# Optimization experiments

Measured on AMD Instinct MI355X. Metric: run time of the kernel, lower is better.

Reference implementation:

```python
import jax, jax.numpy as jnp
import numpy as np

N, DIM, H, E = 50000, 64, 8, 800000
NEG_SLOPE = 0.2


def setup_inputs() -> dict:
    key = jax.random.key(0)
    ks = jax.random.split(key, 6)
    x = jax.random.normal(ks[0], (N, DIM), dtype=jnp.float32)
    edge_index = jax.random.randint(ks[1], (2, E), 0, N, dtype=jnp.int32)
    # glorot-ish scaled params
    W = jax.random.normal(ks[2], (DIM, H * DIM), dtype=jnp.float32) * (1.0 / np.sqrt(DIM))
    att_src = jax.random.normal(ks[3], (H, DIM), dtype=jnp.float32) * (1.0 / np.sqrt(DIM))
    att_dst = jax.random.normal(ks[4], (H, DIM), dtype=jnp.float32) * (1.0 / np.sqrt(DIM))
    bias = jnp.zeros((DIM,), dtype=jnp.float32)
    return {"x": x, "edge_index": edge_index, "W": W, "att_src": att_src, "att_dst": att_dst, "bias": bias}


def reference(x, edge_index, W, att_src, att_dst, bias):
    n = x.shape[0]
    # PyG GATConv default: add self-loops
    loops = jnp.arange(n, dtype=edge_index.dtype)
    src = jnp.concatenate([edge_index[0], loops])  # [E+N]
    dst = jnp.concatenate([edge_index[1], loops])  # [E+N]
    # project: [N, H, C]
    h = (x @ W).reshape(n, H, DIM)
    # per-node attention contributions: [N, H]
    a_src = jnp.einsum("nhc,hc->nh", h, att_src)
    a_dst = jnp.einsum("nhc,hc->nh", h, att_dst)
    # per-edge logits with LeakyReLU: [E+N, H]
    logits = jax.nn.leaky_relu(a_src[src] + a_dst[dst], negative_slope=NEG_SLOPE)
    # segment softmax over incoming edges of each destination node
    seg_max = jax.ops.segment_max(logits, dst, num_segments=n)  # [N, H]
    seg_max = jnp.where(jnp.isfinite(seg_max), seg_max, 0.0)
    e = jnp.exp(logits - seg_max[dst])
    denom = jax.ops.segment_sum(e, dst, num_segments=n)  # [N, H]
    alpha = e / denom[dst]  # every node has a self-loop -> denom > 0
    # weighted messages and scatter-add: [E+N, H, C] -> [N, H, C]
    msg = h[src] * alpha[:, :, None]
    out = jax.ops.segment_sum(msg, dst, num_segments=n)
    # concat=False -> mean over heads, then bias
    return out.mean(axis=1) + bias
```

## Files before the change

### kernel.cpp

```cpp
#include <hip/hip_runtime.h>
#include <hip/hip_bf16.h>

#define NHEAD 8
#define KDIM 64
#define NCOL 512
#define NEG_SLOPE 0.2f
#define BUCKET 64
#define EPT 8

typedef short bf16x8 __attribute__((ext_vector_type(8)));
typedef float f32x4 __attribute__((ext_vector_type(4)));

__device__ inline float leaky(float x) { return fmaxf(x, NEG_SLOPE * x); }
__device__ inline float bf2f(unsigned short u) { return __uint_as_float(((unsigned)u) << 16); }
__device__ inline unsigned short f2bf(float f) {
    unsigned b = __float_as_uint(f);
    b += 0x7FFFu + ((b >> 16) & 1u);
    return (unsigned short)(b >> 16);
}

__global__ void k_wprep(const float* __restrict__ W, const float* __restrict__ att_src,
                        const float* __restrict__ att_dst,
                        float* __restrict__ WsT, float* __restrict__ WdT,
                        unsigned short* __restrict__ Bhi, unsigned short* __restrict__ Blo) {
    int tid = blockIdx.x * 256 + threadIdx.x;
    if (tid < NHEAD * KDIM) {
        int h = tid >> 6, k = tid & 63;
        float ps = 0.f, pd = 0.f;
        const float4* wp = (const float4*)(W + (size_t)k * NCOL + h * KDIM);
        const float4* sp = (const float4*)(att_src + h * KDIM);
        const float4* dp = (const float4*)(att_dst + h * KDIM);
        #pragma unroll
        for (int q = 0; q < KDIM / 4; ++q) {
            float4 wv = wp[q], sv = sp[q], dv = dp[q];
            ps += wv.x * sv.x + wv.y * sv.y + wv.z * sv.z + wv.w * sv.w;
            pd += wv.x * dv.x + wv.y * dv.y + wv.z * dv.z + wv.w * dv.w;
        }
        WsT[h * KDIM + k] = ps;
        WdT[h * KDIM + k] = pd;
    }
    if (tid < 4 * 16 * 64 * 8) {
        int j  = tid & 7;
        int l  = (tid >> 3) & 63;
        int kk = (tid >> 9) & 15;
        int ct = tid >> 13;
        int c  = ct * 16 + (l & 15);
        int hk = kk * 32 + ((l >> 4) << 3) + j;
        int h = hk >> 6, kx = hk & 63;
        float w = W[(size_t)kx * NCOL + h * KDIM + c];
        unsigned short hi = f2bf(w);
        Bhi[tid] = hi;
        Blo[tid] = f2bf(w - bf2f(hi));
    }
}

__global__ void k_xafill(const float* __restrict__ x,
                         const int* __restrict__ src, const int* __restrict__ dst,
                         const float* __restrict__ WsT, const float* __restrict__ WdT,
                         float* __restrict__ asrc, float* __restrict__ adst,
                         unsigned short* __restrict__ xb,
                         int* __restrict__ cur, unsigned short* __restrict__ bucket,
                         int n, int E, int nbx) {
    const int b = blockIdx.x;
    const int t = threadIdx.x;
    if (b < nbx) {
        int i = b * 256 + t;
        if (i >= n * NHEAD) return;
        int node = i >> 3, h = i & 7;
        const float4* xp = (const float4*)(x + (size_t)node * KDIM);
        const float4* sp = (const float4*)(WsT + h * KDIM);
        const float4* dp = (const float4*)(WdT + h * KDIM);
        float ps = 0.f, pd = 0.f;
        float4 kept0 = {0, 0, 0, 0}, kept1 = {0, 0, 0, 0};
        #pragma unroll
        for (int q = 0; q < KDIM / 4; ++q) {
            float4 xv = xp[q], sv = sp[q], dv = dp[q];
            if (q == 2 * h)     kept0 = xv;
            if (q == 2 * h + 1) kept1 = xv;
            ps += xv.x * sv.x + xv.y * sv.y + xv.z * sv.z + xv.w * sv.w;
            pd += xv.x * dv.x + xv.y * dv.y + xv.z * dv.z + xv.w * dv.w;
        }
        asrc[i] = ps;
        adst[i] = pd;
        ushort4 o0, o1;
        o0.x = f2bf(kept0.x); o0.y = f2bf(kept0.y); o0.z = f2bf(kept0.z); o0.w = f2bf(kept0.w);
        o1.x = f2bf(kept1.x); o1.y = f2bf(kept1.y); o1.z = f2bf(kept1.z); o1.w = f2bf(kept1.w);
        ushort4* op = (ushort4*)(xb + (size_t)node * KDIM + h * 8);
        op[0] = o0; op[1] = o1;
    } else {
        long long base = ((long long)(b - nbx) * 256 + t) * EPT;
        if (base + EPT <= E) {
            int4 d0 = *(const int4*)(dst + base);
            int4 d1 = *(const int4*)(dst + base + 4);
            int4 s0 = *(const int4*)(src + base);
            int4 s1 = *(const int4*)(src + base + 4);
            int dd[EPT] = {d0.x, d0.y, d0.z, d0.w, d1.x, d1.y, d1.z, d1.w};
            int ss[EPT] = {s0.x, s0.y, s0.z, s0.w, s1.x, s1.y, s1.z, s1.w};
            int pp[EPT];
            #pragma unroll
            for (int q = 0; q < EPT; ++q) pp[q] = atomicAdd(cur + dd[q], 1);
            #pragma unroll
            for (int q = 0; q < EPT; ++q)
                if (pp[q] < BUCKET)
                    bucket[(size_t)dd[q] * BUCKET + pp[q]] = (unsigned short)ss[q];
        } else {
            for (long long i = base; i < E; ++i) {
                int d = dst[i];
                int p = atomicAdd(cur + d, 1);
                if (p < BUCKET) bucket[(size_t)d * BUCKET + p] = (unsigned short)src[i];
            }
        }
    }
}

__global__ __launch_bounds__(256, 8) void k_aggproj(const unsigned short* __restrict__ bucket,
                                                    const int* __restrict__ cur,
                                                    const float* __restrict__ asrc,
                                                    const float* __restrict__ adst,
                                                    const unsigned short* __restrict__ xb,
                                                    const unsigned short* __restrict__ Bhi,
                                                    const unsigned short* __restrict__ Blo,
                                                    const float* __restrict__ bias,
                                                    float* __restrict__ out, int n) {
    __shared__ __align__(16) unsigned short Yh_l[16][520];

    const int t = threadIdx.x;
    const int w = t >> 6;
    const int lane = t & 63;
    const int base = blockIdx.x * 16;
    const int hg = lane >> 3;
    const int dly = (lane & 7) << 3;

    for (int q = 0; q < 4; ++q) {
        const int row = w * 4 + q;
        int d = base + row;
        if (d >= n) d = n - 1;

        const float myAd = adst[(size_t)d * NHEAD + hg];
        float den = 0.f;
        float y[8];
        #pragma unroll
        for (int i = 0; i < 8; ++i) y[i] = 0.f;

#define PROCU(AV, RW)                                                          \
    {                                                                          \
        float e_ = __expf(leaky((AV) + myAd));                                 \
        den += e_;                                                             \
        uint4 u_ = (RW);                                                       \
        y[0] += e_ * __uint_as_float(u_.x << 16);                              \
        y[1] += e_ * __uint_as_float(u_.x & 0xFFFF0000u);                      \
        y[2] += e_ * __uint_as_float(u_.y << 16);                              \
        y[3] += e_ * __uint_as_float(u_.y & 0xFFFF0000u);                      \
        y[4] += e_ * __uint_as_float(u_.z << 16);                              \
        y[5] += e_ * __uint_as_float(u_.z & 0xFFFF0000u);                      \
        y[6] += e_ * __uint_as_float(u_.w << 16);                              \
        y[7] += e_ * __uint_as_float(u_.w & 0xFFFF0000u);                      \
    }

        int cnt = cur[d];
        cnt = cnt < BUCKET ? cnt : BUCKET;
        int sv = (lane < cnt) ? (int)bucket[(size_t)d * BUCKET + lane] : 0;

        {
            float a = asrc[(size_t)d * NHEAD + hg];
            uint4 r = *(const uint4*)(xb + ((size_t)d << 6) + dly);
            PROCU(a, r)
        }

        int j = 0;
        for (; j + 4 <= cnt; j += 4) {
            int s0 = __shfl(sv, j);
            int s1 = __shfl(sv, j + 1);
            int s2 = __shfl(sv, j + 2);
            int s3 = __shfl(sv, j + 3);
            float a0 = asrc[(size_t)s0 * NHEAD + hg];
            float a1 = asrc[(size_t)s1 * NHEAD + hg];
            float a2 = asrc[(size_t)s2 * NHEAD + hg];
            float a3 = asrc[(size_t)s3 * NHEAD + hg];
            uint4 r0 = *(const uint4*)(xb + ((size_t)s0 << 6) + dly);
            uint4 r1 = *(const uint4*)(xb + ((size_t)s1 << 6) + dly);
            uint4 r2 = *(const uint4*)(xb + ((size_t)s2 << 6) + dly);
            uint4 r3 = *(const uint4*)(xb + ((size_t)s3 << 6) + dly);
            PROCU(a0, r0)
            PROCU(a1, r1)
            PROCU(a2, r2)
            PROCU(a3, r3)
        }
        for (; j < cnt; ++j) {
            int s = __shfl(sv, j);
            float a = asrc[(size_t)s * NHEAD + hg];
            uint4 r = *(const uint4*)(xb + ((size_t)s << 6) + dly);
            PROCU(a, r)
        }
#undef PROCU

        float inv = 1.0f / den;
        ushort4 h0, h1;
        h0.x = f2bf(y[0] * inv); h0.y = f2bf(y[1] * inv);
        h0.z = f2bf(y[2] * inv); h0.w = f2bf(y[3] * inv);
        h1.x = f2bf(y[4] * inv); h1.y = f2bf(y[5] * inv);
        h1.z = f2bf(y[6] * inv); h1.w = f2bf(y[7] * inv);
        unsigned short* yh = &Yh_l[row][hg * KDIM + dly];
        ((ushort4*)yh)[0] = h0; ((ushort4*)yh)[1] = h1;
    }

    __syncthreads();

    const bf16x8* BH = (const bf16x8*)Bhi;
    const bf16x8* BL = (const bf16x8*)Blo;
    const int ar = lane & 15;
    const int ak = (lane >> 4) << 3;

    f32x4 acc = {0.f, 0.f, 0.f, 0.f};
    #pragma unroll
    for (int kk = 0; kk < 16; ++kk) {
        bf16x8 ah = *(const bf16x8*)&Yh_l[ar][kk * 32 + ak];
        bf16x8 bh = BH[(w * 16 + kk) * 64 + lane];
        bf16x8 bl = BL[(w * 16 + kk) * 64 + lane];
        acc = __builtin_amdgcn_mfma_f32_16x16x32_bf16(ah, bh, acc, 0, 0, 0);
        acc = __builtin_amdgcn_mfma_f32_16x16x32_bf16(ah, bl, acc, 0, 0, 0);
    }

    int col = w * 16 + (lane & 15);
    float b = bias[col];
    int rbase = base + ((lane >> 4) << 2);
    #pragma unroll
    for (int r = 0; r < 4; ++r) {
        int rowg = rbase + r;
        if (rowg < n) out[(size_t)rowg * KDIM + col] = acc[r] * 0.125f + b;
    }
}

extern "C" void kernel_launch(void* const* d_in, const int* in_sizes, int n_in,
                              void* d_out, int out_size, void* d_ws, size_t ws_size,
                              hipStream_t stream) {
    const float* x       = (const float*)d_in[0];
    const int*   ei      = (const int*)d_in[1];
    const float* W       = (const float*)d_in[2];
    const float* att_src = (const float*)d_in[3];
    const float* att_dst = (const float*)d_in[4];
    const float* bias    = (const float*)d_in[5];

    const int n = in_sizes[0] / KDIM;
    const int E = in_sizes[1] / 2;
    const int* src = ei;
    const int* dst = ei + E;

    char* w = (char*)d_ws;
    unsigned short* xb  = (unsigned short*)w;  w += (size_t)n * KDIM * 2;
    unsigned short* Bhi = (unsigned short*)w;  w += (size_t)32768 * 2;
    unsigned short* Blo = (unsigned short*)w;  w += (size_t)32768 * 2;
    float* WsT  = (float*)w;                   w += (size_t)NHEAD * KDIM * 4;
    float* WdT  = (float*)w;                   w += (size_t)NHEAD * KDIM * 4;
    float* asrc = (float*)w;                   w += (size_t)n * NHEAD * 4;
    float* adst = (float*)w;                   w += (size_t)n * NHEAD * 4;
    int*   cur  = (int*)w;                     w += (size_t)n * 4;
    unsigned short* bucket = (unsigned short*)w; w += (size_t)n * BUCKET * 2;

    hipMemsetAsync(cur, 0, (size_t)n * 4, stream);

    k_wprep<<<128, 256, 0, stream>>>(W, att_src, att_dst, WsT, WdT, Bhi, Blo);

    const int nbx = (n * NHEAD + 255) / 256;
    const int ethreads = (E + EPT - 1) / EPT;
    const int nbe = (ethreads + 255) / 256;
    k_xafill<<<nbx + nbe, 256, 0, stream>>>(x, src, dst, WsT, WdT, asrc, adst, xb,
                                            cur, bucket, n, E, nbx);

    k_aggproj<<<(n + 15) / 16, 256, 0, stream>>>(bucket, cur, asrc, adst, xb, Bhi, Blo,
                                                 bias, (float*)d_out, n);
}
```

Measured before the change: 156.6 us.

## Fold counter reset into weight prep, dedupe exp per edge, store x as fp16

Removes the separate memset by zeroing the per-node counters inside the weight-prep kernel. The aggregation loop now computes one exp per (edge, head) across lanes and broadcasts it with shuffles, instead of every lane recomputing it for its head. The loop is also unrolled to 8 edges. The gathered x rows are stored as fp16 instead of bf16, which changes the rounding of the messages and adds half-to-float conversions.

```diff
diff --git a/kernel.cpp b/kernel.cpp
--- a/kernel.cpp
+++ b/kernel.cpp
@@ -1,5 +1,6 @@
 #include <hip/hip_runtime.h>
 #include <hip/hip_bf16.h>
+#include <hip/hip_fp16.h>
 
 #define NHEAD 8
 #define KDIM 64
@@ -22,8 +23,10 @@
 __global__ void k_wprep(const float* __restrict__ W, const float* __restrict__ att_src,
                         const float* __restrict__ att_dst,
                         float* __restrict__ WsT, float* __restrict__ WdT,
-                        unsigned short* __restrict__ Bhi, unsigned short* __restrict__ Blo) {
+                        unsigned short* __restrict__ Bhi, unsigned short* __restrict__ Blo,
+                        int* __restrict__ cur, int n) {
     int tid = blockIdx.x * 256 + threadIdx.x;
+    for (int i = tid; i < n; i += 32768) cur[i] = 0;
     if (tid < NHEAD * KDIM) {
         int h = tid >> 6, k = tid & 63;
         float ps = 0.f, pd = 0.f;
@@ -83,8 +86,14 @@
         asrc[i] = ps;
         adst[i] = pd;
         ushort4 o0, o1;
-        o0.x = f2bf(kept0.x); o0.y = f2bf(kept0.y); o0.z = f2bf(kept0.z); o0.w = f2bf(kept0.w);
-        o1.x = f2bf(kept1.x); o1.y = f2bf(kept1.y); o1.z = f2bf(kept1.z); o1.w = f2bf(kept1.w);
+        o0.x = __half_as_ushort(__float2half_rn(kept0.x));
+        o0.y = __half_as_ushort(__float2half_rn(kept0.y));
+        o0.z = __half_as_ushort(__float2half_rn(kept0.z));
+        o0.w = __half_as_ushort(__float2half_rn(kept0.w));
+        o1.x = __half_as_ushort(__float2half_rn(kept1.x));
+        o1.y = __half_as_ushort(__float2half_rn(kept1.y));
+        o1.z = __half_as_ushort(__float2half_rn(kept1.z));
+        o1.w = __half_as_ushort(__float2half_rn(kept1.w));
         ushort4* op = (ushort4*)(xb + (size_t)node * KDIM + h * 8);
         op[0] = o0; op[1] = o1;
     } else {
@@ -129,70 +138,92 @@
     const int lane = t & 63;
     const int base = blockIdx.x * 16;
     const int hg = lane >> 3;
+    const int hLo = lane & 7;
     const int dly = (lane & 7) << 3;
+
+#define PROCU(EV, RW)                                                          \
+    {                                                                          \
+        den += (EV);                                                           \
+        const __half* hx_ = (const __half*)&(RW);                              \
+        y[0] = fmaf(__half2float(hx_[0]), (EV), y[0]);                         \
+        y[1] = fmaf(__half2float(hx_[1]), (EV), y[1]);                         \
+        y[2] = fmaf(__half2float(hx_[2]), (EV), y[2]);                         \
+        y[3] = fmaf(__half2float(hx_[3]), (EV), y[3]);                         \
+        y[4] = fmaf(__half2float(hx_[4]), (EV), y[4]);                         \
+        y[5] = fmaf(__half2float(hx_[5]), (EV), y[5]);                         \
+        y[6] = fmaf(__half2float(hx_[6]), (EV), y[6]);                         \
+        y[7] = fmaf(__half2float(hx_[7]), (EV), y[7]);                         \
+    }
 
     for (int q = 0; q < 4; ++q) {
         const int row = w * 4 + q;
         int d = base + row;
         if (d >= n) d = n - 1;
 
-        const float myAd = adst[(size_t)d * NHEAD + hg];
+        const float adLo = adst[(size_t)d * NHEAD + hLo];
         float den = 0.f;
         float y[8];
         #pragma unroll
         for (int i = 0; i < 8; ++i) y[i] = 0.f;
 
-#define PROCU(AV, RW)                                                          \
-    {                                                                          \
-        float e_ = __expf(leaky((AV) + myAd));                                 \
-        den += e_;                                                             \
-        uint4 u_ = (RW);                                                       \
-        y[0] += e_ * __uint_as_float(u_.x << 16);                              \
-        y[1] += e_ * __uint_as_float(u_.x & 0xFFFF0000u);                      \
-        y[2] += e_ * __uint_as_float(u_.y << 16);                              \
-        y[3] += e_ * __uint_as_float(u_.y & 0xFFFF0000u);                      \
-        y[4] += e_ * __uint_as_float(u_.z << 16);                              \
-        y[5] += e_ * __uint_as_float(u_.z & 0xFFFF0000u);                      \
-        y[6] += e_ * __uint_as_float(u_.w << 16);                              \
-        y[7] += e_ * __uint_as_float(u_.w & 0xFFFF0000u);                      \
-    }
-
         int cnt = cur[d];
         cnt = cnt < BUCKET ? cnt : BUCKET;
         int sv = (lane < cnt) ? (int)bucket[(size_t)d * BUCKET + lane] : 0;
 
         {
-            float a = asrc[(size_t)d * NHEAD + hg];
+            float asLo = asrc[(size_t)d * NHEAD + hLo];
+            float evs = __expf(leaky(asLo + adLo));
+            float e = __shfl(evs, hg);
             uint4 r = *(const uint4*)(xb + ((size_t)d << 6) + dly);
-            PROCU(a, r)
+            PROCU(e, r)
         }
 
         int j = 0;
-        for (; j + 4 <= cnt; j += 4) {
+        for (; j + 8 <= cnt; j += 8) {
+            int sb = __shfl(sv, j + (lane >> 3));
+            float ab = asrc[(size_t)sb * NHEAD + hLo];
+            float ev = __expf(leaky(ab + adLo));
             int s0 = __shfl(sv, j);
             int s1 = __shfl(sv, j + 1);
             int s2 = __shfl(sv, j + 2);
             int s3 = __shfl(sv, j + 3);
-            float a0 = asrc[(size_t)s0 * NHEAD + hg];
-            float a1 = asrc[(size_t)s1 * NHEAD + hg];
-            float a2 = asrc[(size_t)s2 * NHEAD + hg];
-            float a3 = asrc[(size_t)s3 * NHEAD + hg];
+            int s4 = __shfl(sv, j + 4);
+            int s5 = __shfl(sv, j + 5);
+            int s6 = __shfl(sv, j + 6);
+            int s7 = __shfl(sv, j + 7);
             uint4 r0 = *(const uint4*)(xb + ((size_t)s0 << 6) + dly);
             uint4 r1 = *(const uint4*)(xb + ((size_t)s1 << 6) + dly);
             uint4 r2 = *(const uint4*)(xb + ((size_t)s2 << 6) + dly);
             uint4 r3 = *(const uint4*)(xb + ((size_t)s3 << 6) + dly);
-            PROCU(a0, r0)
-            PROCU(a1, r1)
-            PROCU(a2, r2)
-            PROCU(a3, r3)
+            uint4 r4 = *(const uint4*)(xb + ((size_t)s4 << 6) + dly);
+            uint4 r5 = *(const uint4*)(xb + ((size_t)s5 << 6) + dly);
+            uint4 r6 = *(const uint4*)(xb + ((size_t)s6 << 6) + dly);
+            uint4 r7 = *(const uint4*)(xb + ((size_t)s7 << 6) + dly);
+            float e0 = __shfl(ev, 0 * 8 + hg);
+            float e1 = __shfl(ev, 1 * 8 + hg);
+            float e2 = __shfl(ev, 2 * 8 + hg);
+            float e3 = __shfl(ev, 3 * 8 + hg);
+            float e4 = __shfl(ev, 4 * 8 + hg);
+            float e5 = __shfl(ev, 5 * 8 + hg);
+            float e6 = __shfl(ev, 6 * 8 + hg);
+            float e7 = __shfl(ev, 7 * 8 + hg);
+            PROCU(e0, r0)
+            PROCU(e1, r1)
+            PROCU(e2, r2)
+            PROCU(e3, r3)
+            PROCU(e4, r4)
+            PROCU(e5, r5)
+            PROCU(e6, r6)
+            PROCU(e7, r7)
         }
         for (; j < cnt; ++j) {
             int s = __shfl(sv, j);
-            float a = asrc[(size_t)s * NHEAD + hg];
+            float a = asrc[(size_t)s * NHEAD + hLo];
+            float evt = __expf(leaky(a + adLo));
+            float e = __shfl(evt, hg);
             uint4 r = *(const uint4*)(xb + ((size_t)s << 6) + dly);
-            PROCU(a, r)
-        }
-#undef PROCU
+            PROCU(e, r)
+        }
 
         float inv = 1.0f / den;
         ushort4 h0, h1;
@@ -203,6 +234,7 @@
         unsigned short* yh = &Yh_l[row][hg * KDIM + dly];
         ((ushort4*)yh)[0] = h0; ((ushort4*)yh)[1] = h1;
     }
+#undef PROCU
 
     __syncthreads();
 
@@ -257,9 +289,7 @@
     int*   cur  = (int*)w;                     w += (size_t)n * 4;
     unsigned short* bucket = (unsigned short*)w; w += (size_t)n * BUCKET * 2;
 
-    hipMemsetAsync(cur, 0, (size_t)n * 4, stream);
-
-    k_wprep<<<128, 256, 0, stream>>>(W, att_src, att_dst, WsT, WdT, Bhi, Blo);
+    k_wprep<<<128, 256, 0, stream>>>(W, att_src, att_dst, WsT, WdT, Bhi, Blo, cur, n);
 
     const int nbx = (n * NHEAD + 255) / 256;
     const int ethreads = (E + EPT - 1) / EPT;
```

New measurement: 178.6 us. 1.14x slower.
